# Kernel tuning notes

Measured on AMD Instinct MI355X. Metric: run time of the kernel, lower is better.

The kernel has to match this reference:

```python
import jax, jax.numpy as jnp
import numpy as np

SEQ_LEN = 256

# static upper-triangular pair indices (i <= j), ordered exactly like the
# original loop: for i in range(S): for j in range(i, S)
_I, _J = np.triu_indices(SEQ_LEN)
IDX_I = jnp.asarray(_I)  # (P,) with P = S*(S+1)/2
IDX_J = jnp.asarray(_J)


def setup_inputs() -> dict:
    key = jax.random.key(0)
    k1, k2, k3 = jax.random.split(key, 3)
    batch, seq_len, hidden = 4, SEQ_LEN, 768
    seq_hiddens = jax.random.normal(k1, (batch, seq_len, hidden), dtype=jnp.float32)
    # nn.Linear(2h, h): weight (h, 2h) in torch; store transposed (2h, h)
    W = jax.random.normal(k2, (2 * hidden, hidden), dtype=jnp.float32) * (1.0 / np.sqrt(2 * hidden))
    b = jax.random.normal(k3, (hidden,), dtype=jnp.float32) * 0.01
    return {"seq_hiddens": seq_hiddens, "W": W, "b": b}


def reference(seq_hiddens, W, b):
    # cat([h_i, h_j]) @ W + b == h @ W1 (at i) + h @ W2 (at j) + b.
    # Project once per position (S*h GEMM), then gather into the triangle —
    # avoids materializing the (B, P, 2h) concat tensor.
    h = seq_hiddens.shape[-1]
    W1, W2 = W[:h], W[h:]                       # (h, h) each
    left = jnp.einsum('bsh,hd->bsd', seq_hiddens, W1)   # (B, S, h)
    right = jnp.einsum('bsh,hd->bsd', seq_hiddens, W2)  # (B, S, h)
    # (B, P, h): pair (i, j) gets left[:, i] + right[:, j] + b
    return jnp.tanh(left[:, IDX_I, :] + right[:, IDX_J, :] + b)
```

## Files before the change

kernel.cpp:

```cpp
#include <hip/hip_runtime.h>
#include <stdint.h>

typedef short  s16x8 __attribute__((ext_vector_type(8)));
typedef float  f32x4 __attribute__((ext_vector_type(4)));

#define HIDDEN 768
#define SEQ    256
#define BATCH  4
#define NPAIR  32896

__device__ inline unsigned short f2bf(float f) {
    unsigned int u = __float_as_uint(f);
    u += 0x7FFFu + ((u >> 16) & 1u);
    return (unsigned short)(u >> 16);
}

__global__ void cast_x(const float* __restrict__ X, unsigned short* __restrict__ Xb) {
    int idx = blockIdx.x * 256 + threadIdx.x;
    f32x4 v = ((const f32x4*)X)[idx];
    ushort4 o;
    o.x = f2bf(v[0]); o.y = f2bf(v[1]); o.z = f2bf(v[2]); o.w = f2bf(v[3]);
    ((ushort4*)Xb)[idx] = o;
}

__global__ void transpose_w(const float* __restrict__ W, unsigned short* __restrict__ Wt) {
    __shared__ float tile[32][33];
    const float*     Wh  = W  + (size_t)blockIdx.z * HIDDEN * HIDDEN;
    unsigned short*  Wth = Wt + (size_t)blockIdx.z * HIDDEN * HIDDEN;
    int tx = threadIdx.x, ty = threadIdx.y;
    int k0 = blockIdx.x * 32, n0 = blockIdx.y * 32;
#pragma unroll
    for (int r = 0; r < 4; ++r)
        tile[ty + 8*r][tx] = Wh[(size_t)(k0 + ty + 8*r) * HIDDEN + n0 + tx];
    __syncthreads();
#pragma unroll
    for (int r = 0; r < 4; ++r)
        Wth[(size_t)(n0 + ty + 8*r) * HIDDEN + k0 + tx] = f2bf(tile[tx][ty + 8*r]);
}

__global__ __launch_bounds__(256) void gemm_lr(const unsigned short* __restrict__ Xb,
                                               const unsigned short* __restrict__ Wt,
                                               const float* __restrict__ bias,
                                               float* __restrict__ L,
                                               float* __restrict__ R) {
    __shared__ unsigned short Als[64][32];
    __shared__ unsigned short Bls[64][32];
    const int t    = threadIdx.x;
    const int m0   = blockIdx.y * 64;
    const int nblk = blockIdx.x;
    const bool isL = nblk < 12;
    const int n0   = (isL ? nblk : nblk - 12) * 64;

    const int w = t >> 6, lane = t & 63, quad = lane >> 4, l16 = lane & 15;
    const int wm = (w & 1) * 32, wn = (w >> 1) * 32;

    f32x4 acc00 = {0,0,0,0}, acc01 = {0,0,0,0}, acc10 = {0,0,0,0}, acc11 = {0,0,0,0};

    const int row = t >> 2, seg = t & 3;
    const uint4* Ag = (const uint4*)Xb + (size_t)(m0 + row) * 96 + seg;
    const uint4* Bg = (const uint4*)(Wt + (size_t)nblk * 64 * HIDDEN) + (size_t)row * 96 + seg;
    uint4* Alw = (uint4*)(&Als[0][0]) + t;
    uint4* Blw = (uint4*)(&Bls[0][0]) + t;

    uint4 av = Ag[0], bv = Bg[0];
#pragma unroll 1
    for (int kc = 0; kc < 24; ++kc) {
        *Alw = av; *Blw = bv;
        __syncthreads();
        if (kc < 23) { av = Ag[(kc + 1) * 4]; bv = Bg[(kc + 1) * 4]; }
        s16x8 a0 = *(const s16x8*)&Als[wm      + l16][quad * 8];
        s16x8 a1 = *(const s16x8*)&Als[wm + 16 + l16][quad * 8];
        s16x8 b0 = *(const s16x8*)&Bls[wn      + l16][quad * 8];
        s16x8 b1 = *(const s16x8*)&Bls[wn + 16 + l16][quad * 8];
        acc00 = __builtin_amdgcn_mfma_f32_16x16x32_bf16(a0, b0, acc00, 0, 0, 0);
        acc01 = __builtin_amdgcn_mfma_f32_16x16x32_bf16(a0, b1, acc01, 0, 0, 0);
        acc10 = __builtin_amdgcn_mfma_f32_16x16x32_bf16(a1, b0, acc10, 0, 0, 0);
        acc11 = __builtin_amdgcn_mfma_f32_16x16x32_bf16(a1, b1, acc11, 0, 0, 0);
        __syncthreads();
    }

    float* dst = isL ? L : R;
    const f32x4 accs[2][2] = {{acc00, acc01}, {acc10, acc11}};
#pragma unroll
    for (int mi = 0; mi < 2; ++mi)
#pragma unroll
        for (int ni = 0; ni < 2; ++ni) {
            const int n = n0 + wn + ni * 16 + l16;
            const float badd = isL ? bias[n] : 0.0f;
#pragma unroll
            for (int r = 0; r < 4; ++r) {
                const int m = m0 + wm + mi * 16 + quad * 4 + r;
                dst[(size_t)m * HIDDEN + n] = accs[mi][ni][r] + badd;
            }
        }
}

__global__ __launch_bounds__(192) void expand(const float* __restrict__ L,
                                              const float* __restrict__ R,
                                              float* __restrict__ out) {
    const int bid = blockIdx.x, b = blockIdx.y, t = threadIdx.x;
    const int q  = (bid & 7) * (8224 / 8) + (bid >> 3);
    const int p0 = q * 4;

    int i = (int)(0.5f * (513.0f - sqrtf(263169.0f - 8.0f * (float)p0)));
    if (i < 0) i = 0; if (i > 255) i = 255;
    int s = (i * (513 - i)) >> 1;
    while (s > p0) { --i; s = (i * (513 - i)) >> 1; }
    while (p0 - s >= 256 - i) { s += 256 - i; ++i; }
    int j = i + (p0 - s);

    const float* Lb = L + (size_t)b * 256 * HIDDEN;
    const float* Rb = R + (size_t)b * 256 * HIDDEN;
    f32x4* Ob = (f32x4*)out + ((size_t)b * NPAIR + p0) * 192 + t;

    f32x4 lv[4], rv[4];
    int ii = i, jj = j;
#pragma unroll
    for (int u = 0; u < 4; ++u) {
        lv[u] = ((const f32x4*)(Lb + (size_t)ii * HIDDEN))[t];
        rv[u] = ((const f32x4*)(Rb + (size_t)jj * HIDDEN))[t];
        if (jj < 255) { ++jj; } else { ++ii; jj = ii; }
    }
#pragma unroll
    for (int u = 0; u < 4; ++u) {
        f32x4 o;
#pragma unroll
        for (int c = 0; c < 4; ++c) {
            const float x = lv[u][c] + rv[u][c];
            const float e = __expf(2.0f * x);
            o[c] = 1.0f - 2.0f * __builtin_amdgcn_rcpf(e + 1.0f);
        }
        __builtin_nontemporal_store(o, Ob + (size_t)u * 192);
    }
}

extern "C" void kernel_launch(void* const* d_in, const int* in_sizes, int n_in,
                              void* d_out, int out_size, void* d_ws, size_t ws_size,
                              hipStream_t stream) {
    const float* X = (const float*)d_in[0];
    const float* W = (const float*)d_in[1];
    const float* b = (const float*)d_in[2];
    float* out = (float*)d_out;

    char* ws = (char*)d_ws;
    unsigned short* Xb = (unsigned short*)(ws);
    unsigned short* Wt = (unsigned short*)(ws + 1572864);
    float*          L  = (float*)(ws + 3932160);
    float*          R  = (float*)(ws + 7077888);

    hipLaunchKernelGGL(cast_x,      dim3(768),          dim3(256),   0, stream, X, Xb);
    hipLaunchKernelGGL(transpose_w, dim3(24, 24, 2),    dim3(32, 8), 0, stream, W, Wt);
    hipLaunchKernelGGL(gemm_lr,     dim3(24, 16),       dim3(256),   0, stream, Xb, Wt, b, L, R);
    hipLaunchKernelGGL(expand,      dim3(8224, BATCH),  dim3(192),   0, stream, L, R, out);
}
```

Measured before the change: 409.6 us.

## Tile expand kernel into 4x4 pair blocks over the triangle

```diff
diff --git a/kernel.cpp b/kernel.cpp
--- a/kernel.cpp
+++ b/kernel.cpp
@@ -8,6 +8,7 @@
 #define SEQ    256
 #define BATCH  4
 #define NPAIR  32896
+#define NTILE  2080
 
 __device__ inline unsigned short f2bf(float f) {
     unsigned int u = __float_as_uint(f);
@@ -95,42 +96,52 @@
         }
 }
 
+__device__ inline f32x4 tanh4(f32x4 l, f32x4 r) {
+    f32x4 o;
+#pragma unroll
+    for (int c = 0; c < 4; ++c) {
+        const float x = l[c] + r[c];
+        const float e = __expf(2.0f * x);
+        o[c] = 1.0f - 2.0f * __builtin_amdgcn_rcpf(e + 1.0f);
+    }
+    return o;
+}
+
 __global__ __launch_bounds__(192) void expand(const float* __restrict__ L,
                                               const float* __restrict__ R,
                                               float* __restrict__ out) {
     const int bid = blockIdx.x, b = blockIdx.y, t = threadIdx.x;
-    const int q  = (bid & 7) * (8224 / 8) + (bid >> 3);
-    const int p0 = q * 4;
+    const int q = (bid & 7) * (NTILE / 8) + (bid >> 3);
 
-    int i = (int)(0.5f * (513.0f - sqrtf(263169.0f - 8.0f * (float)p0)));
-    if (i < 0) i = 0; if (i > 255) i = 255;
-    int s = (i * (513 - i)) >> 1;
-    while (s > p0) { --i; s = (i * (513 - i)) >> 1; }
-    while (p0 - s >= 256 - i) { s += 256 - i; ++i; }
-    int j = i + (p0 - s);
+    int ti = (int)(0.5f * (129.0f - sqrtf(16641.0f - 8.0f * (float)q)));
+    if (ti < 0) ti = 0; if (ti > 63) ti = 63;
+    int s = (ti * (129 - ti)) >> 1;
+    while (s > q) { --ti; s = (ti * (129 - ti)) >> 1; }
+    while (q - s >= 64 - ti) { s += 64 - ti; ++ti; }
+    const int tj = ti + (q - s);
 
+    const int i0 = ti * 4, j0 = tj * 4;
     const float* Lb = L + (size_t)b * 256 * HIDDEN;
     const float* Rb = R + (size_t)b * 256 * HIDDEN;
-    f32x4* Ob = (f32x4*)out + ((size_t)b * NPAIR + p0) * 192 + t;
 
     f32x4 lv[4], rv[4];
-    int ii = i, jj = j;
+#pragma unroll
+    for (int u = 0; u < 4; ++u)
+        lv[u] = ((const f32x4*)(Lb + (size_t)(i0 + u) * HIDDEN))[t];
+#pragma unroll
+    for (int v = 0; v < 4; ++v)
+        rv[v] = ((const f32x4*)(Rb + (size_t)(j0 + v) * HIDDEN))[t];
+
 #pragma unroll
     for (int u = 0; u < 4; ++u) {
-        lv[u] = ((const f32x4*)(Lb + (size_t)ii * HIDDEN))[t];
-        rv[u] = ((const f32x4*)(Rb + (size_t)jj * HIDDEN))[t];
-        if (jj < 255) { ++jj; } else { ++ii; jj = ii; }
-    }
+        const int i = i0 + u;
+        const long pb = (long)((i * (513 - i)) >> 1) + (j0 - i);
+        f32x4* Op = (f32x4*)out + ((size_t)b * NPAIR + pb) * 192 + t;
 #pragma unroll
-    for (int u = 0; u < 4; ++u) {
-        f32x4 o;
-#pragma unroll
-        for (int c = 0; c < 4; ++c) {
-            const float x = lv[u][c] + rv[u][c];
-            const float e = __expf(2.0f * x);
-            o[c] = 1.0f - 2.0f * __builtin_amdgcn_rcpf(e + 1.0f);
+        for (int v = 0; v < 4; ++v) {
+            if (j0 + v >= i)
+                __builtin_nontemporal_store(tanh4(lv[u], rv[v]), Op + (size_t)v * 192);
         }
-        __builtin_nontemporal_store(o, Ob + (size_t)u * 192);
     }
 }
 
@@ -151,5 +162,5 @@
     hipLaunchKernelGGL(cast_x,      dim3(768),          dim3(256),   0, stream, X, Xb);
     hipLaunchKernelGGL(transpose_w, dim3(24, 24, 2),    dim3(32, 8), 0, stream, W, Wt);
     hipLaunchKernelGGL(gemm_lr,     dim3(24, 16),       dim3(256),   0, stream, Xb, Wt, b, L, R);
-    hipLaunchKernelGGL(expand,      dim3(8224, BATCH),  dim3(192),   0, stream, L, R, out);
+    hipLaunchKernelGGL(expand,      dim3(NTILE, BATCH), dim3(192),   0, stream, L, R, out);
 }
```

After: 420.6 us. 2.7% more time.
